# Optimization experiments

Hardware: AMD Instinct MI355X
Metric: run time of the kernel (lower is better)

Reference implementation:

```python
import jax, jax.numpy as jnp
import numpy as np

EPS = 1e-8  # torch F.cosine_similarity eps


def _cosine_logits(latent, codebook):
    # latent: [N, D], codebook: [K, D] -> [N, K]
    ln = jnp.maximum(jnp.linalg.norm(latent, axis=-1, keepdims=True), EPS)   # [N,1]
    cn = jnp.maximum(jnp.linalg.norm(codebook, axis=-1, keepdims=True), EPS)  # [K,1]
    # Equivalent to broadcast N x K x D cosine sim, computed as one GEMM.
    return jnp.einsum('nd,kd->nk', latent, codebook) / (ln * cn.T)


def setup_inputs() -> dict:
    key = jax.random.key(0)
    k1, k2, k3 = jax.random.split(key, 3)
    N, K, D = 131072, 1024, 256
    latent_representation = jax.random.normal(k1, (N, D), dtype=jnp.float32)
    codebook = jax.random.normal(k2, (K, D), dtype=jnp.float32)
    temperature = jnp.float32(1.0)
    # uniform in (0,1) so -log(-log(u)) is finite
    noise_u = jax.random.uniform(k3, (N, K), dtype=jnp.float32, minval=1e-6, maxval=1.0)
    return {
        'latent_representation': latent_representation,
        'noise_u': noise_u,
        'codebook': codebook,
        'temperature': temperature,
    }


def reference(latent_representation, noise_u, codebook, temperature):
    logits = _cosine_logits(latent_representation, codebook) / temperature
    gumbel = -jnp.log(-jnp.log(noise_u))
    logits = logits + gumbel
    # softmax is monotone, so argmax(softmax(logits)) == argmax(logits)
    hard_indices = jnp.argmax(logits, axis=-1)           # [N]
    quantized = jnp.take(codebook, hard_indices, axis=0)  # [N, D]
    return quantized
```

## Files before the change

### kernel.cpp

```cpp
#include <hip/hip_runtime.h>
#include <math.h>

#define D_DIM 256
#define K_CB  1024
#define EPS   1e-8f

typedef _Float16 half4_t __attribute__((ext_vector_type(4)));
typedef _Float16 half8_t __attribute__((ext_vector_type(8)));
typedef float    f32x4   __attribute__((ext_vector_type(4)));

__device__ __forceinline__ void split2(const float4 v, half4_t& h, half4_t& l)
{
    h[0] = (_Float16)v.x; h[1] = (_Float16)v.y;
    h[2] = (_Float16)v.z; h[3] = (_Float16)v.w;
    l[0] = (_Float16)((v.x - (float)h[0]) * 2048.0f);
    l[1] = (_Float16)((v.y - (float)h[1]) * 2048.0f);
    l[2] = (_Float16)((v.z - (float)h[2]) * 2048.0f);
    l[3] = (_Float16)((v.w - (float)h[3]) * 2048.0f);
}

__global__ __launch_bounds__(256) void qnorms_kernel(
    const float* __restrict__ latent,
    const float* __restrict__ codebook,
    const float* __restrict__ temp,
    float* __restrict__ scales,
    int N)
{
    const int w = blockIdx.x * 4 + (threadIdx.x >> 6);
    const int lane = threadIdx.x & 63;
    if (w >= N + K_CB) return;
    const float* src = (w < K_CB) ? (codebook + (size_t)w * D_DIM)
                                  : (latent + (size_t)(w - K_CB) * D_DIM);
    float4 v = reinterpret_cast<const float4*>(src)[lane];
    float ss = v.x * v.x + v.y * v.y + v.z * v.z + v.w * v.w;
#pragma unroll
    for (int off = 32; off > 0; off >>= 1) ss += __shfl_down(ss, off, 64);
    if (lane == 0) {
        const float inv = 1.0f / fmaxf(sqrtf(ss), EPS);
        scales[w] = (w < K_CB) ? inv : inv / temp[0];
    }
}

__global__ __launch_bounds__(256, 1) void qmain_kernel(
    const float* __restrict__ latent,
    const float* __restrict__ noise,
    const float* __restrict__ codebook,
    const float* __restrict__ scales,
    float* __restrict__ out,
    int N)
{
    __shared__ __align__(16) _Float16 A0s[64 * 256];
    __shared__ __align__(16) _Float16 A1s[64 * 256];
    __shared__ __align__(16) _Float16 Bs[2][2][256 * 32];
    __shared__ __align__(16) float cscale_s[K_CB];
    __shared__ float vmax_s[2][64];
    __shared__ int   vidx_s[2][64];
    __shared__ int   idx_s[64];

    const int tid  = threadIdx.x;
    const int row0 = blockIdx.x * 64;
    const int wid  = tid >> 6;
    const int lane = tid & 63;
    const int wr   = wid >> 1;
    const int wc   = wid & 1;
    const int c16  = lane & 15;
    const int g    = lane >> 4;

    {
        const int f4   = tid & 63;
        const int rsub = tid >> 6;
        const int d0   = f4 * 4;
#pragma unroll
        for (int p = 0; p < 16; ++p) {
            const int row = p * 4 + rsub;
            const float4 v = reinterpret_cast<const float4*>(
                latent + (size_t)(row0 + row) * D_DIM)[f4];
            half4_t h0, h1; split2(v, h0, h1);
            const int idx = row * 256 + (d0 ^ ((row & 7) << 3));
            *reinterpret_cast<half4_t*>(&A0s[idx]) = h0;
            *reinterpret_cast<half4_t*>(&A1s[idx]) = h1;
        }
    }
    {
        const float4 v = reinterpret_cast<const float4*>(scales)[tid];
        reinterpret_cast<float4*>(cscale_s)[tid] = v;
    }

    const int colb = tid >> 3;
    const int dg   = tid & 7;

#pragma unroll
    for (int p = 0; p < 8; ++p) {
        const int col = p * 32 + colb;
        const float4 v = *reinterpret_cast<const float4*>(
            codebook + (size_t)col * D_DIM + dg * 4);
        half4_t h0, h1; split2(v, h0, h1);
        const int idx = col * 32 + ((dg * 4) ^ (((col >> 1) & 3) << 3));
        *reinterpret_cast<half4_t*>(&Bs[0][0][idx]) = h0;
        *reinterpret_cast<half4_t*>(&Bs[0][1][idx]) = h1;
    }
    __syncthreads();

    float rscale[2][4];
#pragma unroll
    for (int rt = 0; rt < 2; ++rt)
#pragma unroll
        for (int j = 0; j < 4; ++j)
            rscale[rt][j] = scales[K_CB + row0 + wr * 32 + rt * 16 + g * 4 + j];

    float rmax[2][4];
    int   ridx[2][4];
#pragma unroll
    for (int rt = 0; rt < 2; ++rt)
#pragma unroll
        for (int j = 0; j < 4; ++j) { rmax[rt][j] = -INFINITY; ridx[rt][j] = 0x7fffffff; }

    f32x4 acc_hi[2][8], acc_mid[2][8];

    for (int ct = 0; ct < 4; ++ct) {
#pragma unroll
        for (int rt = 0; rt < 2; ++rt)
#pragma unroll
            for (int t = 0; t < 8; ++t)
#pragma unroll
                for (int q = 0; q < 4; ++q) { acc_hi[rt][t][q] = 0.0f; acc_mid[rt][t][q] = 0.0f; }

        for (int ds = 0; ds < 8; ++ds) {
            const int s   = ct * 8 + ds;
            const int buf = s & 1;
            const bool pf = (s < 31);
            float4 pv[8];
            if (pf) {
                const int sn  = s + 1;
                const int cb2 = (sn >> 3) * 256;
                const int db2 = (sn & 7) * 32;
#pragma unroll
                for (int p = 0; p < 8; ++p) {
                    const int col = p * 32 + colb;
                    pv[p] = *reinterpret_cast<const float4*>(
                        codebook + (size_t)(cb2 + col) * D_DIM + db2 + dg * 4);
                }
            }

            const int dA = ds * 32 + g * 8;
            half8_t a0[2], a1[2];
#pragma unroll
            for (int rt = 0; rt < 2; ++rt) {
                const int arow = wr * 32 + rt * 16 + c16;
                const int aidx = arow * 256 + (dA ^ ((arow & 7) << 3));
                a0[rt] = *reinterpret_cast<const half8_t*>(&A0s[aidx]);
                a1[rt] = *reinterpret_cast<const half8_t*>(&A1s[aidx]);
            }
#pragma unroll
            for (int t = 0; t < 8; ++t) {
                const int col  = wc * 128 + t * 16 + c16;
                const int bidx = col * 32 + ((g * 8) ^ (((col >> 1) & 3) << 3));
                const half8_t b0 = *reinterpret_cast<const half8_t*>(&Bs[buf][0][bidx]);
                const half8_t b1 = *reinterpret_cast<const half8_t*>(&Bs[buf][1][bidx]);
#pragma unroll
                for (int rt = 0; rt < 2; ++rt) {
                    acc_hi[rt][t]  = __builtin_amdgcn_mfma_f32_16x16x32_f16(
                        a0[rt], b0, acc_hi[rt][t], 0, 0, 0);
                    acc_mid[rt][t] = __builtin_amdgcn_mfma_f32_16x16x32_f16(
                        a1[rt], b0, acc_mid[rt][t], 0, 0, 0);
                    acc_mid[rt][t] = __builtin_amdgcn_mfma_f32_16x16x32_f16(
                        a0[rt], b1, acc_mid[rt][t], 0, 0, 0);
                }
            }

            if (pf) {
#pragma unroll
                for (int p = 0; p < 8; ++p) {
                    const int col = p * 32 + colb;
                    half4_t h0, h1; split2(pv[p], h0, h1);
                    const int idx = col * 32 + ((dg * 4) ^ (((col >> 1) & 3) << 3));
                    *reinterpret_cast<half4_t*>(&Bs[buf ^ 1][0][idx]) = h0;
                    *reinterpret_cast<half4_t*>(&Bs[buf ^ 1][1][idx]) = h1;
                }
            }
            __syncthreads();
        }

#pragma unroll
        for (int rt = 0; rt < 2; ++rt) {
#pragma unroll
            for (int j = 0; j < 4; ++j) {
                const int rowg = row0 + wr * 32 + rt * 16 + g * 4 + j;
                const float rs = rscale[rt][j];
                const float* nrow = noise + (size_t)rowg * K_CB;
                float v  = rmax[rt][j];
                int   vi = ridx[rt][j];
#pragma unroll
                for (int t = 0; t < 8; ++t) {
                    const int colg = ct * 256 + wc * 128 + t * 16 + c16;
                    const float u   = nrow[colg];
                    const float gum = -logf(-logf(u));
                    const float dot = acc_hi[rt][t][j] + acc_mid[rt][t][j] * (1.0f / 2048.0f);
                    const float l   = fmaf(dot * rs, cscale_s[colg], gum);
                    if (l > v || (l == v && colg < vi)) { v = l; vi = colg; }
                }
                rmax[rt][j] = v;
                ridx[rt][j] = vi;
            }
        }
    }

#pragma unroll
    for (int rt = 0; rt < 2; ++rt)
#pragma unroll
        for (int j = 0; j < 4; ++j) {
            float v  = rmax[rt][j];
            int   vi = ridx[rt][j];
#pragma unroll
            for (int off = 1; off < 16; off <<= 1) {
                const float ov = __shfl_xor(v, off, 64);
                const int   oi = __shfl_xor(vi, off, 64);
                if (ov > v || (ov == v && oi < vi)) { v = ov; vi = oi; }
            }
            if (c16 == 0) {
                const int rloc = wr * 32 + rt * 16 + g * 4 + j;
                vmax_s[wc][rloc] = v;
                vidx_s[wc][rloc] = vi;
            }
        }
    __syncthreads();
    if (tid < 64) {
        float v0 = vmax_s[0][tid]; int i0 = vidx_s[0][tid];
        const float v1 = vmax_s[1][tid]; const int i1 = vidx_s[1][tid];
        if (v1 > v0 || (v1 == v0 && i1 < i0)) { i0 = i1; }
        idx_s[tid] = i0;
    }
    __syncthreads();

    {
        const int l2 = tid & 63;
        const int rr = tid >> 6;
#pragma unroll
        for (int p = 0; p < 16; ++p) {
            const int row = rr * 16 + p;
            const int idx = idx_s[row];
            const float4 v =
                reinterpret_cast<const float4*>(codebook + (size_t)idx * D_DIM)[l2];
            reinterpret_cast<float4*>(out + (size_t)(row0 + row) * D_DIM)[l2] = v;
        }
    }
}

extern "C" void kernel_launch(void* const* d_in, const int* in_sizes, int n_in,
                              void* d_out, int out_size, void* d_ws, size_t ws_size,
                              hipStream_t stream)
{
    const float* latent   = (const float*)d_in[0];
    const float* noise    = (const float*)d_in[1];
    const float* codebook = (const float*)d_in[2];
    const float* temp     = (const float*)d_in[3];
    float* out    = (float*)d_out;
    float* scales = (float*)d_ws;
    const int N = in_sizes[0] / D_DIM;

    const int nw = (N + K_CB + 3) / 4;
    qnorms_kernel<<<nw, 256, 0, stream>>>(latent, codebook, temp, scales, N);
    qmain_kernel<<<N / 64, 256, 0, stream>>>(latent, noise, codebook, scales, out, N);
}
```

Measured before the change: 1.805 ms.

## Precompute normalized split-fp16 codebook image and read B fragments from global

Adds a pre-pass that normalizes the codebook, splits it into hi/lo fp16 halves and stores them in a fragment-ready layout in workspace. The main kernel then loads B fragments straight from global (L2-resident) instead of staging them through double-buffered LDS with per-step syncs. Latent rows are pre-scaled by their inverse norm and temperature before splitting, so the per-element scale multiply in the epilogue is dropped. Each wave now covers all 64 rows by a 64-column slice, and occupancy is raised to 2 blocks per CU. The trade is extra global/L2 traffic for B fragments with no LDS reuse across waves, plus a slightly different rounding order because normalization happens before the fp16 split.

```diff
diff --git a/kernel.cpp b/kernel.cpp
--- a/kernel.cpp
+++ b/kernel.cpp
@@ -21,50 +21,71 @@
 
 __global__ __launch_bounds__(256) void qnorms_kernel(
     const float* __restrict__ latent,
-    const float* __restrict__ codebook,
     const float* __restrict__ temp,
     float* __restrict__ scales,
     int N)
 {
     const int w = blockIdx.x * 4 + (threadIdx.x >> 6);
     const int lane = threadIdx.x & 63;
-    if (w >= N + K_CB) return;
-    const float* src = (w < K_CB) ? (codebook + (size_t)w * D_DIM)
-                                  : (latent + (size_t)(w - K_CB) * D_DIM);
-    float4 v = reinterpret_cast<const float4*>(src)[lane];
+    if (w >= N) return;
+    float4 v = reinterpret_cast<const float4*>(latent + (size_t)w * D_DIM)[lane];
     float ss = v.x * v.x + v.y * v.y + v.z * v.z + v.w * v.w;
 #pragma unroll
     for (int off = 32; off > 0; off >>= 1) ss += __shfl_down(ss, off, 64);
-    if (lane == 0) {
-        const float inv = 1.0f / fmaxf(sqrtf(ss), EPS);
-        scales[w] = (w < K_CB) ? inv : inv / temp[0];
-    }
-}
-
-__global__ __launch_bounds__(256, 1) void qmain_kernel(
+    if (lane == 0)
+        scales[w] = 1.0f / (fmaxf(sqrtf(ss), EPS) * temp[0]);
+}
+
+__global__ __launch_bounds__(256) void cbsplit_kernel(
+    const float* __restrict__ codebook,
+    _Float16* __restrict__ b0img,
+    _Float16* __restrict__ b1img)
+{
+    const int k    = blockIdx.x * 4 + (threadIdx.x >> 6);
+    const int lane = threadIdx.x & 63;
+    float4 v = reinterpret_cast<const float4*>(codebook + (size_t)k * D_DIM)[lane];
+    float ss = v.x * v.x + v.y * v.y + v.z * v.z + v.w * v.w;
+#pragma unroll
+    for (int off = 1; off < 64; off <<= 1) ss += __shfl_xor(ss, off, 64);
+    const float inv = 1.0f / fmaxf(sqrtf(ss), EPS);
+    v.x *= inv; v.y *= inv; v.z *= inv; v.w *= inv;
+    half4_t h0, h1; split2(v, h0, h1);
+
+    const int d  = lane * 4;
+    const int ct = k >> 8, cl = k & 255;
+    const int s  = ct * 8 + (d >> 5);
+    const int g  = (d >> 3) & 3;
+    const size_t ha = ((size_t)(s * 4 + g) * 256 + cl) * 8 + (d & 7);
+    *reinterpret_cast<half4_t*>(b0img + ha) = h0;
+    *reinterpret_cast<half4_t*>(b1img + ha) = h1;
+}
+
+__global__ __launch_bounds__(256, 2) void qmain_kernel(
     const float* __restrict__ latent,
     const float* __restrict__ noise,
     const float* __restrict__ codebook,
     const float* __restrict__ scales,
+    const _Float16* __restrict__ b0img,
+    const _Float16* __restrict__ b1img,
     float* __restrict__ out,
     int N)
 {
     __shared__ __align__(16) _Float16 A0s[64 * 256];
     __shared__ __align__(16) _Float16 A1s[64 * 256];
-    __shared__ __align__(16) _Float16 Bs[2][2][256 * 32];
-    __shared__ __align__(16) float cscale_s[K_CB];
-    __shared__ float vmax_s[2][64];
-    __shared__ int   vidx_s[2][64];
+    __shared__ float scale_s[64];
+    __shared__ float vmax_s[4][64];
+    __shared__ int   vidx_s[4][64];
     __shared__ int   idx_s[64];
 
     const int tid  = threadIdx.x;
     const int row0 = blockIdx.x * 64;
-    const int wid  = tid >> 6;
+    const int wc   = tid >> 6;
     const int lane = tid & 63;
-    const int wr   = wid >> 1;
-    const int wc   = wid & 1;
     const int c16  = lane & 15;
     const int g    = lane >> 4;
+
+    if (tid < 64) scale_s[tid] = scales[row0 + tid];
+    __syncthreads();
 
     {
         const int f4   = tid & 63;
@@ -73,131 +94,88 @@
 #pragma unroll
         for (int p = 0; p < 16; ++p) {
             const int row = p * 4 + rsub;
-            const float4 v = reinterpret_cast<const float4*>(
+            float4 v = reinterpret_cast<const float4*>(
                 latent + (size_t)(row0 + row) * D_DIM)[f4];
+            const float sc = scale_s[row];
+            v.x *= sc; v.y *= sc; v.z *= sc; v.w *= sc;
             half4_t h0, h1; split2(v, h0, h1);
             const int idx = row * 256 + (d0 ^ ((row & 7) << 3));
             *reinterpret_cast<half4_t*>(&A0s[idx]) = h0;
             *reinterpret_cast<half4_t*>(&A1s[idx]) = h1;
         }
     }
-    {
-        const float4 v = reinterpret_cast<const float4*>(scales)[tid];
-        reinterpret_cast<float4*>(cscale_s)[tid] = v;
-    }
-
-    const int colb = tid >> 3;
-    const int dg   = tid & 7;
-
-#pragma unroll
-    for (int p = 0; p < 8; ++p) {
-        const int col = p * 32 + colb;
-        const float4 v = *reinterpret_cast<const float4*>(
-            codebook + (size_t)col * D_DIM + dg * 4);
-        half4_t h0, h1; split2(v, h0, h1);
-        const int idx = col * 32 + ((dg * 4) ^ (((col >> 1) & 3) << 3));
-        *reinterpret_cast<half4_t*>(&Bs[0][0][idx]) = h0;
-        *reinterpret_cast<half4_t*>(&Bs[0][1][idx]) = h1;
-    }
-    __syncthreads();
-
-    float rscale[2][4];
-#pragma unroll
-    for (int rt = 0; rt < 2; ++rt)
-#pragma unroll
-        for (int j = 0; j < 4; ++j)
-            rscale[rt][j] = scales[K_CB + row0 + wr * 32 + rt * 16 + g * 4 + j];
-
-    float rmax[2][4];
-    int   ridx[2][4];
-#pragma unroll
-    for (int rt = 0; rt < 2; ++rt)
+    __syncthreads();
+
+    float rmax[4][4];
+    int   ridx[4][4];
+#pragma unroll
+    for (int rt = 0; rt < 4; ++rt)
 #pragma unroll
         for (int j = 0; j < 4; ++j) { rmax[rt][j] = -INFINITY; ridx[rt][j] = 0x7fffffff; }
 
-    f32x4 acc_hi[2][8], acc_mid[2][8];
+    const int boff8 = g * 256 + wc * 64 + c16;
 
     for (int ct = 0; ct < 4; ++ct) {
-#pragma unroll
-        for (int rt = 0; rt < 2; ++rt)
-#pragma unroll
-            for (int t = 0; t < 8; ++t)
-#pragma unroll
-                for (int q = 0; q < 4; ++q) { acc_hi[rt][t][q] = 0.0f; acc_mid[rt][t][q] = 0.0f; }
+        f32x4 acc_hi[4][4], acc_mid[4][4];
+#pragma unroll
+        for (int rt = 0; rt < 4; ++rt)
+#pragma unroll
+            for (int t = 0; t < 4; ++t) {
+                acc_hi[rt][t]  = (f32x4){0.f, 0.f, 0.f, 0.f};
+                acc_mid[rt][t] = (f32x4){0.f, 0.f, 0.f, 0.f};
+            }
 
         for (int ds = 0; ds < 8; ++ds) {
-            const int s   = ct * 8 + ds;
-            const int buf = s & 1;
-            const bool pf = (s < 31);
-            float4 pv[8];
-            if (pf) {
-                const int sn  = s + 1;
-                const int cb2 = (sn >> 3) * 256;
-                const int db2 = (sn & 7) * 32;
-#pragma unroll
-                for (int p = 0; p < 8; ++p) {
-                    const int col = p * 32 + colb;
-                    pv[p] = *reinterpret_cast<const float4*>(
-                        codebook + (size_t)(cb2 + col) * D_DIM + db2 + dg * 4);
-                }
+            const int s = ct * 8 + ds;
+            const _Float16* bp0 = b0img + (size_t)s * 8192;
+            const _Float16* bp1 = b1img + (size_t)s * 8192;
+
+            half8_t bh[4], bl[4];
+#pragma unroll
+            for (int t = 0; t < 4; ++t) {
+                bh[t] = *reinterpret_cast<const half8_t*>(bp0 + (size_t)(boff8 + t * 16) * 8);
+                bl[t] = *reinterpret_cast<const half8_t*>(bp1 + (size_t)(boff8 + t * 16) * 8);
             }
 
             const int dA = ds * 32 + g * 8;
-            half8_t a0[2], a1[2];
-#pragma unroll
-            for (int rt = 0; rt < 2; ++rt) {
-                const int arow = wr * 32 + rt * 16 + c16;
+            half8_t a0[4], a1[4];
+#pragma unroll
+            for (int rt = 0; rt < 4; ++rt) {
+                const int arow = rt * 16 + c16;
                 const int aidx = arow * 256 + (dA ^ ((arow & 7) << 3));
                 a0[rt] = *reinterpret_cast<const half8_t*>(&A0s[aidx]);
                 a1[rt] = *reinterpret_cast<const half8_t*>(&A1s[aidx]);
             }
 #pragma unroll
-            for (int t = 0; t < 8; ++t) {
-                const int col  = wc * 128 + t * 16 + c16;
-                const int bidx = col * 32 + ((g * 8) ^ (((col >> 1) & 3) << 3));
-                const half8_t b0 = *reinterpret_cast<const half8_t*>(&Bs[buf][0][bidx]);
-                const half8_t b1 = *reinterpret_cast<const half8_t*>(&Bs[buf][1][bidx]);
-#pragma unroll
-                for (int rt = 0; rt < 2; ++rt) {
+            for (int t = 0; t < 4; ++t)
+#pragma unroll
+                for (int rt = 0; rt < 4; ++rt) {
                     acc_hi[rt][t]  = __builtin_amdgcn_mfma_f32_16x16x32_f16(
-                        a0[rt], b0, acc_hi[rt][t], 0, 0, 0);
+                        a0[rt], bh[t], acc_hi[rt][t], 0, 0, 0);
                     acc_mid[rt][t] = __builtin_amdgcn_mfma_f32_16x16x32_f16(
-                        a1[rt], b0, acc_mid[rt][t], 0, 0, 0);
+                        a1[rt], bh[t], acc_mid[rt][t], 0, 0, 0);
                     acc_mid[rt][t] = __builtin_amdgcn_mfma_f32_16x16x32_f16(
-                        a0[rt], b1, acc_mid[rt][t], 0, 0, 0);
+                        a0[rt], bl[t], acc_mid[rt][t], 0, 0, 0);
                 }
-            }
-
-            if (pf) {
-#pragma unroll
-                for (int p = 0; p < 8; ++p) {
-                    const int col = p * 32 + colb;
-                    half4_t h0, h1; split2(pv[p], h0, h1);
-                    const int idx = col * 32 + ((dg * 4) ^ (((col >> 1) & 3) << 3));
-                    *reinterpret_cast<half4_t*>(&Bs[buf ^ 1][0][idx]) = h0;
-                    *reinterpret_cast<half4_t*>(&Bs[buf ^ 1][1][idx]) = h1;
-                }
-            }
-            __syncthreads();
-        }
-
-#pragma unroll
-        for (int rt = 0; rt < 2; ++rt) {
+        }
+
+#pragma unroll
+        for (int rt = 0; rt < 4; ++rt) {
 #pragma unroll
             for (int j = 0; j < 4; ++j) {
-                const int rowg = row0 + wr * 32 + rt * 16 + g * 4 + j;
-                const float rs = rscale[rt][j];
-                const float* nrow = noise + (size_t)rowg * K_CB;
+                const int rowg = row0 + rt * 16 + g * 4 + j;
+                const float* nrow = noise + (size_t)rowg * K_CB + ct * 256;
                 float v  = rmax[rt][j];
                 int   vi = ridx[rt][j];
 #pragma unroll
-                for (int t = 0; t < 8; ++t) {
-                    const int colg = ct * 256 + wc * 128 + t * 16 + c16;
-                    const float u   = nrow[colg];
+                for (int t = 0; t < 4; ++t) {
+                    const int cloc = wc * 64 + t * 16 + c16;
+                    const float u   = nrow[cloc];
                     const float gum = -logf(-logf(u));
-                    const float dot = acc_hi[rt][t][j] + acc_mid[rt][t][j] * (1.0f / 2048.0f);
-                    const float l   = fmaf(dot * rs, cscale_s[colg], gum);
-                    if (l > v || (l == v && colg < vi)) { v = l; vi = colg; }
+                    const float l   = acc_hi[rt][t][j]
+                                    + acc_mid[rt][t][j] * (1.0f / 2048.0f) + gum;
+                    const int cidx = ct * 256 + cloc;
+                    if (l > v || (l == v && cidx < vi)) { v = l; vi = cidx; }
                 }
                 rmax[rt][j] = v;
                 ridx[rt][j] = vi;
@@ -206,29 +184,33 @@
     }
 
 #pragma unroll
-    for (int rt = 0; rt < 2; ++rt)
+    for (int rt = 0; rt < 4; ++rt)
 #pragma unroll
         for (int j = 0; j < 4; ++j) {
             float v  = rmax[rt][j];
             int   vi = ridx[rt][j];
 #pragma unroll
             for (int off = 1; off < 16; off <<= 1) {
-                const float ov = __shfl_xor(v, off, 64);
-                const int   oi = __shfl_xor(vi, off, 64);
+                const float ov = __shfl_xor(v, off, 16);
+                const int   oi = __shfl_xor(vi, off, 16);
                 if (ov > v || (ov == v && oi < vi)) { v = ov; vi = oi; }
             }
             if (c16 == 0) {
-                const int rloc = wr * 32 + rt * 16 + g * 4 + j;
+                const int rloc = rt * 16 + g * 4 + j;
                 vmax_s[wc][rloc] = v;
                 vidx_s[wc][rloc] = vi;
             }
         }
     __syncthreads();
     if (tid < 64) {
-        float v0 = vmax_s[0][tid]; int i0 = vidx_s[0][tid];
-        const float v1 = vmax_s[1][tid]; const int i1 = vidx_s[1][tid];
-        if (v1 > v0 || (v1 == v0 && i1 < i0)) { i0 = i1; }
-        idx_s[tid] = i0;
+        float v = vmax_s[0][tid]; int vi = vidx_s[0][tid];
+#pragma unroll
+        for (int w = 1; w < 4; ++w) {
+            const float ov = vmax_s[w][tid];
+            const int   oi = vidx_s[w][tid];
+            if (ov > v || (ov == v && oi < vi)) { v = ov; vi = oi; }
+        }
+        idx_s[tid] = vi;
     }
     __syncthreads();
 
@@ -257,8 +239,11 @@
     float* out    = (float*)d_out;
     float* scales = (float*)d_ws;
     const int N = in_sizes[0] / D_DIM;
-
-    const int nw = (N + K_CB + 3) / 4;
-    qnorms_kernel<<<nw, 256, 0, stream>>>(latent, codebook, temp, scales, N);
-    qmain_kernel<<<N / 64, 256, 0, stream>>>(latent, noise, codebook, scales, out, N);
-}
+    _Float16* b0img = (_Float16*)(scales + N);
+    _Float16* b1img = b0img + 32 * 8192;
+
+    qnorms_kernel<<<(N + 3) / 4, 256, 0, stream>>>(latent, temp, scales, N);
+    cbsplit_kernel<<<K_CB / 4, 256, 0, stream>>>(codebook, b0img, b1img);
+    qmain_kernel<<<N / 64, 256, 0, stream>>>(latent, noise, codebook, scales,
+                                             b0img, b1img, out, N);
+}
```

Result: slower. 1.880 ms (+4.1%).
